# Kernel optimization log

Measured on AMD Instinct MI355X. Metric: run time of the kernel, lower is better.

Reference implementation:

```python
import jax, jax.numpy as jnp
import numpy as np

N = 100000   # nodes
E = 1280000  # edges (avg degree ~12.8)
D = 64       # feature / hidden channels


def _init_linear(key, fan_in, fan_out):
    # Kaiming-uniform-ish init like torch Linear
    bound = 1.0 / np.sqrt(fan_in)
    return jax.random.uniform(key, (fan_in, fan_out), minval=-bound, maxval=bound)


def setup_inputs() -> dict:
    key = jax.random.key(0)
    ks = jax.random.split(key, 16)
    inp = {
        "x": jax.random.normal(ks[0], (N, D), dtype=jnp.float32),
        "edge_index": jax.random.randint(ks[1], (2, E), 0, N, dtype=jnp.int32),
        "edge_weight": jax.random.uniform(ks[2], (E,), dtype=jnp.float32),
        "batch": jnp.zeros((N,), dtype=jnp.int32),
    }
    # GraphConv params per layer: lin_rel (weight+bias) applied to aggregated
    # neighbor sum, lin_root (weight, no bias) applied to the node itself.
    for i, k in zip((1, 2, 3), range(3, 12, 3)):
        inp[f"W_rel{i}"] = _init_linear(ks[k], D, D)
        inp[f"b_rel{i}"] = jnp.zeros((D,), dtype=jnp.float32)
        inp[f"W_root{i}"] = _init_linear(ks[k + 1], D, D)
    return inp


def _graph_conv(x, src, dst, w, W_rel, b_rel, W_root):
    # message: w_ij * x_j, aggregated (sum) at target nodes
    msg = w[:, None] * x[src]                                  # [E, D]
    agg = jax.ops.segment_sum(msg, dst, num_segments=N)       # [N, D]
    return agg @ W_rel + b_rel + x @ W_root                   # [N, D]


def reference(x, edge_index, edge_weight, batch,
              W_rel1, b_rel1, W_root1,
              W_rel2, b_rel2, W_root2,
              W_rel3, b_rel3, W_root3):
    src, dst = edge_index[0], edge_index[1]
    h = jax.nn.relu(_graph_conv(x, src, dst, edge_weight, W_rel1, b_rel1, W_root1))
    h = jax.nn.relu(_graph_conv(h, src, dst, edge_weight, W_rel2, b_rel2, W_root2))
    h = _graph_conv(h, src, dst, edge_weight, W_rel3, b_rel3, W_root3)
    return h
```

## Files before the change

### kernel.cpp

```cpp
#include <hip/hip_runtime.h>
#include <hip/hip_bf16.h>

#define NN 100000
#define NE 1280000
#define DD 64
#define RSHIFT 9
#define NRANGE 196
#define NPAD (NRANGE * 512)
#define RCAP 8192
#define RPSTRIDE 513

typedef __attribute__((ext_vector_type(8))) short bf16x8;
typedef __attribute__((ext_vector_type(4))) float f32x4;

static __device__ __forceinline__ unsigned short f2bf(float f) {
    __hip_bfloat16 h = __float2bfloat16(f);
    return *reinterpret_cast<unsigned short*>(&h);
}

__global__ __launch_bounds__(256) void f32_to_bf16_kernel(
    const float* __restrict__ in, unsigned short* __restrict__ out)
{
    int i = (blockIdx.x * 256 + threadIdx.x) * 4;
    float4 v = *(const float4*)(in + i);
    ushort4 o;
    o.x = f2bf(v.x); o.y = f2bf(v.y); o.z = f2bf(v.z); o.w = f2bf(v.w);
    *(ushort4*)(out + i) = o;
}

__global__ __launch_bounds__(256) void bpack_kernel(
    const float* __restrict__ Wrel1, const float* __restrict__ Wroot1,
    const float* __restrict__ Wrel2, const float* __restrict__ Wroot2,
    const float* __restrict__ Wrel3, const float* __restrict__ Wroot3,
    unsigned short* __restrict__ Bp, int* __restrict__ gcur)
{
    int L = blockIdx.x;
    int tid = threadIdx.x;
    if (L == 3) {
        if (tid < NRANGE) gcur[tid] = tid * RCAP;
        return;
    }
    const float* Wrel  = (L == 0) ? Wrel1  : (L == 1) ? Wrel2  : Wrel3;
    const float* Wroot = (L == 0) ? Wroot1 : (L == 1) ? Wroot2 : Wroot3;
    int wv = tid >> 6, lane = tid & 63, quad = lane >> 4, m16 = lane & 15;
    int n = wv * 16 + m16;
    unsigned short* o = Bp + (size_t)L * 4 * 256 * 8;
#pragma unroll
    for (int t = 0; t < 4; ++t)
#pragma unroll
        for (int j = 0; j < 8; ++j) {
            int k = t * 32 + quad * 8 + j;
            float wval = (k < 64) ? Wrel[k * 64 + n] : Wroot[(k - 64) * 64 + n];
            o[((size_t)t * 256 + tid) * 8 + j] = f2bf(wval);
        }
}

__global__ __launch_bounds__(512) void p1_bin_kernel(
    const int* __restrict__ src, const int* __restrict__ dst,
    const float* __restrict__ w, int* __restrict__ gcur,
    int2* __restrict__ ecoarse)
{
    __shared__ int2 stage[2048];
    __shared__ unsigned char sbkt[2048];
    __shared__ int cnt[NRANGE], ofs[NRANGE], gpos[NRANGE];
    __shared__ int wsum[4];

    int tid = threadIdx.x;
    int e0 = blockIdx.x * 2048 + tid * 4;
    int4   s4 = *(const int4*)(src + e0);
    int4   d4 = *(const int4*)(dst + e0);
    float4 w4 = *(const float4*)(w + e0);

    if (tid < NRANGE) cnt[tid] = 0;
    __syncthreads();

    int ss[4] = {s4.x, s4.y, s4.z, s4.w};
    int dd[4] = {d4.x, d4.y, d4.z, d4.w};
    float ww[4] = {w4.x, w4.y, w4.z, w4.w};
    int b[4], p[4];
#pragma unroll
    for (int i = 0; i < 4; ++i) {
        b[i] = dd[i] >> RSHIFT;
        p[i] = atomicAdd(&cnt[b[i]], 1);
    }
    __syncthreads();

    int sum = 0, v = 0;
    if (tid < NRANGE) {
        v = cnt[tid];
        int lane6 = tid & 63;
        sum = v;
#pragma unroll
        for (int o = 1; o < 64; o <<= 1) {
            int t = __shfl_up(sum, o);
            if (lane6 >= o) sum += t;
        }
        if (lane6 == 63 || tid == NRANGE - 1) wsum[tid >> 6] = sum;
        ofs[tid] = sum - v;
    }
    __syncthreads();
    if (tid < NRANGE) {
        int wid = tid >> 6;
        int pre = 0;
#pragma unroll
        for (int k = 0; k < 3; ++k) pre += (k < wid) ? wsum[k] : 0;
        ofs[tid] += pre;
        if (v > 0) gpos[tid] = atomicAdd(&gcur[tid], v);
    }
    __syncthreads();

#pragma unroll
    for (int i = 0; i < 4; ++i) {
        int slot = ofs[b[i]] + p[i];
        stage[slot] = make_int2(ss[i] | ((dd[i] & 511) << 17), __float_as_int(ww[i]));
        sbkt[slot] = (unsigned char)b[i];
    }
    __syncthreads();

#pragma unroll
    for (int u = 0; u < 4; ++u) {
        int j = tid + u * 512;
        int bb = sbkt[j];
        ecoarse[gpos[bb] + (j - ofs[bb])] = stage[j];
    }
}

__global__ __launch_bounds__(1024) void p2_place_kernel(
    const int2* __restrict__ ecoarse, const int* __restrict__ gcur,
    int* __restrict__ rowp, int2* __restrict__ ebuf)
{
    __shared__ int cnt[512];
    __shared__ int wsum[8];
    int r = blockIdx.x, tid = threadIdx.x;
    int beg = r * RCAP;
    int end = gcur[r];

    if (tid < 512) cnt[tid] = 0;
    __syncthreads();

    for (int j = beg + tid; j < end; j += 1024) {
        int2 rec = ecoarse[j];
        atomicAdd(&cnt[(rec.x >> 17) & 511], 1);
    }
    __syncthreads();

    int v = 0, sum = 0;
    if (tid < 512) {
        v = cnt[tid]; sum = v;
        int lane6 = tid & 63;
#pragma unroll
        for (int o = 1; o < 64; o <<= 1) {
            int t = __shfl_up(sum, o);
            if (lane6 >= o) sum += t;
        }
        if (lane6 == 63) wsum[tid >> 6] = sum;
    }
    __syncthreads();
    if (tid < 512) {
        int wid = tid >> 6;
        int pre = 0;
#pragma unroll
        for (int k = 0; k < 7; ++k) pre += (k < wid) ? wsum[k] : 0;
        int ex = beg + pre + sum - v;
        rowp[r * RPSTRIDE + tid] = ex;
        cnt[tid] = ex;
    }
    if (tid == 0) rowp[r * RPSTRIDE + 512] = end;
    __syncthreads();

    for (int j = beg + tid; j < end; j += 1024) {
        int2 rec = ecoarse[j];
        int dl = (rec.x >> 17) & 511;
        int pp = atomicAdd(&cnt[dl], 1);
        ebuf[pp] = make_int2((rec.x & 0x1FFFF) << 7, rec.y);
    }
}

template <bool RELU, bool OUT32>
__global__ __launch_bounds__(512) void fused_layer_kernel(
    const unsigned short* __restrict__ hb,
    const int* __restrict__ rowp,
    const int2* __restrict__ ebuf,
    const unsigned short* __restrict__ Bp,
    const float* __restrict__ brel,
    void* __restrict__ outp)
{
    __shared__ __align__(16) unsigned int AstW[4 * 256];
    __shared__ __align__(16) int2 seW[8][64];

    int tid = threadIdx.x;
    int lane = tid & 63;
    int wv = tid >> 6;
    int half = lane >> 5;
    int ch = lane & 31;
    int base = blockIdx.x * 16;
    int node = base + wv * 2 + half;
    int rr = base >> 9;

    const char* __restrict__ hbase = (const char*)hb;
    unsigned chB = (unsigned)ch * 4;

    bf16x8 bfrag[4];
    float bias = 0.f;
    if (wv < 4) {
#pragma unroll
        for (int t2 = 0; t2 < 4; ++t2)
            bfrag[t2] = *(const bf16x8*)(Bp + ((size_t)t2 * 256 + tid) * 8);
        bias = brel[(wv << 4) | (lane & 15)];
    }

    unsigned rootp = *(const unsigned*)(hbase + (size_t)node * 128 + chB);

    int beg = rowp[node + rr];
    int end = rowp[node + rr + 1];
    int deg = end - beg;

    float aL[4] = {0.f, 0.f, 0.f, 0.f};
    float aH[4] = {0.f, 0.f, 0.f, 0.f};

    for (int c = 0; c < deg; c += 32) {
        int nsl = deg - c; if (nsl > 32) nsl = 32;
        {
            int j = c + ch;
            bool ok = j < deg;
            int2 e = ebuf[beg + (ok ? j : (deg - 1))];
            if (!ok) e.y = 0;
            seW[wv][half * 32 + ch] = e;
        }
        for (int s0 = 0; s0 < nsl; s0 += 16) {
#pragma unroll
            for (int i = 0; i < 16; ++i) {
                int2 rec = seW[wv][half * 32 + s0 + i];
                float w = __int_as_float(rec.y);
                unsigned v = *(const unsigned*)(hbase + ((unsigned)rec.x + chB));
                aL[i & 3] = fmaf(w, __uint_as_float(v << 16), aL[i & 3]);
                aH[i & 3] = fmaf(w, __uint_as_float(v & 0xFFFF0000u), aH[i & 3]);
            }
        }
    }
    float accL = (aL[0] + aL[1]) + (aL[2] + aL[3]);
    float accH = (aH[0] + aH[1]) + (aH[2] + aH[3]);

    int m = wv * 2 + half;
    int t = ch >> 4, q = (ch >> 2) & 3, jj = ch & 3;
    unsigned pack = ((unsigned)f2bf(accH) << 16) | (unsigned)f2bf(accL);
    AstW[t * 256 + (q * 16 + m) * 4 + jj] = pack;
    AstW[(2 + t) * 256 + (q * 16 + m) * 4 + jj] = rootp;
    __syncthreads();

    if (wv < 4) {
        int quad = lane >> 4, m16 = lane & 15;
        int n = wv * 16 + m16;
        f32x4 cacc = {0.f, 0.f, 0.f, 0.f};
#pragma unroll
        for (int t2 = 0; t2 < 4; ++t2) {
            bf16x8 a = *(const bf16x8*)&AstW[t2 * 256 + lane * 4];
            cacc = __builtin_amdgcn_mfma_f32_16x16x32_bf16(a, bfrag[t2], cacc, 0, 0, 0);
        }
#pragma unroll
        for (int reg = 0; reg < 4; ++reg) {
            int row = quad * 4 + reg;
            size_t onode = (size_t)base + row;
            float v2 = cacc[reg] + bias;
            if (RELU) v2 = fmaxf(v2, 0.f);
            if (OUT32) ((float*)outp)[onode * DD + n] = v2;
            else       ((unsigned short*)outp)[onode * DD + n] = f2bf(v2);
        }
    }
}

extern "C" void kernel_launch(void* const* d_in, const int* in_sizes, int n_in,
                              void* d_out, int out_size, void* d_ws, size_t ws_size,
                              hipStream_t stream)
{
    const float* x     = (const float*)d_in[0];
    const int*   ei    = (const int*)d_in[1];
    const float* w     = (const float*)d_in[2];
    const float* Wrel1 = (const float*)d_in[4];
    const float* brel1 = (const float*)d_in[5];
    const float* Wroot1= (const float*)d_in[6];
    const float* Wrel2 = (const float*)d_in[7];
    const float* brel2 = (const float*)d_in[8];
    const float* Wroot2= (const float*)d_in[9];
    const float* Wrel3 = (const float*)d_in[10];
    const float* brel3 = (const float*)d_in[11];
    const float* Wroot3= (const float*)d_in[12];

    float* out = (float*)d_out;

    char* ws = (char*)d_ws;
    int2*  ebuf    = (int2*)ws;                ws += (size_t)NRANGE * RCAP * 8;
    int2*  ecoarse = (int2*)ws;
    unsigned short* xb  = (unsigned short*)ws; ws += (size_t)NRANGE * RCAP * 8;
    unsigned short* hb1 = (unsigned short*)ws; ws += (size_t)NPAD * DD * 2;
    unsigned short* hb2 = (unsigned short*)ws; ws += (size_t)NPAD * DD * 2;
    int*   rowp  = (int*)ws;                   ws += (size_t)(NRANGE * RPSTRIDE + 16) * 4;
    int*   gcur  = (int*)ws;                   ws += (size_t)256 * 4;
    unsigned short* Bp = (unsigned short*)ws;

    const int* src = ei;
    const int* dst = ei + NE;

    bpack_kernel<<<4, 256, 0, stream>>>(Wrel1, Wroot1, Wrel2, Wroot2,
                                        Wrel3, Wroot3, Bp, gcur);
    p1_bin_kernel<<<625, 512, 0, stream>>>(src, dst, w, gcur, ecoarse);
    p2_place_kernel<<<NRANGE, 1024, 0, stream>>>(ecoarse, gcur, rowp, ebuf);

    f32_to_bf16_kernel<<<6250, 256, 0, stream>>>(x, xb);

    fused_layer_kernel<true, false><<<NN / 16, 512, 0, stream>>>(
        xb, rowp, ebuf, Bp, brel1, hb1);
    fused_layer_kernel<true, false><<<NN / 16, 512, 0, stream>>>(
        hb1, rowp, ebuf, Bp + (size_t)4 * 256 * 8, brel2, hb2);
    fused_layer_kernel<false, true><<<NN / 16, 512, 0, stream>>>(
        hb2, rowp, ebuf, Bp + (size_t)8 * 256 * 8, brel3, out);
}
```

Measured before the change: 249.7 us.

## Process two nodes per half-wave and split MFMA epilogue across all eight waves

Result: slower. 277.3 us (+11.0%).

```diff
diff --git a/kernel.cpp b/kernel.cpp
--- a/kernel.cpp
+++ b/kernel.cpp
@@ -186,81 +186,98 @@
     void* __restrict__ outp)
 {
     __shared__ __align__(16) unsigned int AstW[4 * 256];
-    __shared__ __align__(16) int2 seW[8][64];
+    __shared__ __align__(16) int2 seW[8][2][64];
 
     int tid = threadIdx.x;
     int lane = tid & 63;
     int wv = tid >> 6;
     int half = lane >> 5;
     int ch = lane & 31;
-    int base = blockIdx.x * 16;
-    int node = base + wv * 2 + half;
+    int base = blockIdx.x * 32;
+    int m = wv * 2 + half;
+    int nodeA = base + m;
+    int nodeB = base + 16 + m;
     int rr = base >> 9;
 
     const char* __restrict__ hbase = (const char*)hb;
     unsigned chB = (unsigned)ch * 4;
 
+    int ti = wv >> 2, wv4 = wv & 3;
+    int quad = lane >> 4, m16 = lane & 15;
+
     bf16x8 bfrag[4];
-    float bias = 0.f;
-    if (wv < 4) {
-#pragma unroll
-        for (int t2 = 0; t2 < 4; ++t2)
-            bfrag[t2] = *(const bf16x8*)(Bp + ((size_t)t2 * 256 + tid) * 8);
-        bias = brel[(wv << 4) | (lane & 15)];
-    }
-
-    unsigned rootp = *(const unsigned*)(hbase + (size_t)node * 128 + chB);
-
-    int beg = rowp[node + rr];
-    int end = rowp[node + rr + 1];
-    int deg = end - beg;
-
-    float aL[4] = {0.f, 0.f, 0.f, 0.f};
-    float aH[4] = {0.f, 0.f, 0.f, 0.f};
-
-    for (int c = 0; c < deg; c += 32) {
-        int nsl = deg - c; if (nsl > 32) nsl = 32;
+#pragma unroll
+    for (int t2 = 0; t2 < 4; ++t2)
+        bfrag[t2] = *(const bf16x8*)(Bp + ((size_t)t2 * 256 + (tid & 255)) * 8);
+    float bias = brel[(wv4 << 4) | m16];
+    const char* rrow = hbase + (size_t)(base + ti * 16 + m16) * 128 + quad * 16;
+    bf16x8 aroot0 = *(const bf16x8*)(rrow);
+    bf16x8 aroot1 = *(const bf16x8*)(rrow + 64);
+
+    int begA = rowp[nodeA + rr];
+    int degA = rowp[nodeA + rr + 1] - begA;
+    int begB = rowp[nodeB + rr];
+    int degB = rowp[nodeB + rr + 1] - begB;
+    int dM = degA > degB ? degA : degB;
+
+    float aLA[4] = {0.f,0.f,0.f,0.f}, aHA[4] = {0.f,0.f,0.f,0.f};
+    float aLB[4] = {0.f,0.f,0.f,0.f}, aHB[4] = {0.f,0.f,0.f,0.f};
+
+    for (int c = 0; c < dM; c += 32) {
         {
             int j = c + ch;
-            bool ok = j < deg;
-            int2 e = ebuf[beg + (ok ? j : (deg - 1))];
-            if (!ok) e.y = 0;
-            seW[wv][half * 32 + ch] = e;
-        }
+            int ja = j < degA ? j : (degA - 1); if (ja < 0) ja = 0;
+            int jb = j < degB ? j : (degB - 1); if (jb < 0) jb = 0;
+            int2 eA = ebuf[begA + ja];
+            int2 eB = ebuf[begB + jb];
+            if (j >= degA) eA.y = 0;
+            if (j >= degB) eB.y = 0;
+            seW[wv][0][half * 32 + ch] = eA;
+            seW[wv][1][half * 32 + ch] = eB;
+        }
+        int nsl = dM - c; if (nsl > 32) nsl = 32;
         for (int s0 = 0; s0 < nsl; s0 += 16) {
 #pragma unroll
             for (int i = 0; i < 16; ++i) {
-                int2 rec = seW[wv][half * 32 + s0 + i];
-                float w = __int_as_float(rec.y);
-                unsigned v = *(const unsigned*)(hbase + ((unsigned)rec.x + chB));
-                aL[i & 3] = fmaf(w, __uint_as_float(v << 16), aL[i & 3]);
-                aH[i & 3] = fmaf(w, __uint_as_float(v & 0xFFFF0000u), aH[i & 3]);
+                int2 rA = seW[wv][0][half * 32 + s0 + i];
+                int2 rB = seW[wv][1][half * 32 + s0 + i];
+                float wA = __int_as_float(rA.y);
+                float wB = __int_as_float(rB.y);
+                unsigned vA = *(const unsigned*)(hbase + ((unsigned)rA.x + chB));
+                unsigned vB = *(const unsigned*)(hbase + ((unsigned)rB.x + chB));
+                aLA[i & 3] = fmaf(wA, __uint_as_float(vA << 16), aLA[i & 3]);
+                aHA[i & 3] = fmaf(wA, __uint_as_float(vA & 0xFFFF0000u), aHA[i & 3]);
+                aLB[i & 3] = fmaf(wB, __uint_as_float(vB << 16), aLB[i & 3]);
+                aHB[i & 3] = fmaf(wB, __uint_as_float(vB & 0xFFFF0000u), aHB[i & 3]);
             }
         }
     }
-    float accL = (aL[0] + aL[1]) + (aL[2] + aL[3]);
-    float accH = (aH[0] + aH[1]) + (aH[2] + aH[3]);
-
-    int m = wv * 2 + half;
+    float accLA = (aLA[0] + aLA[1]) + (aLA[2] + aLA[3]);
+    float accHA = (aHA[0] + aHA[1]) + (aHA[2] + aHA[3]);
+    float accLB = (aLB[0] + aLB[1]) + (aLB[2] + aLB[3]);
+    float accHB = (aHB[0] + aHB[1]) + (aHB[2] + aHB[3]);
+
     int t = ch >> 4, q = (ch >> 2) & 3, jj = ch & 3;
-    unsigned pack = ((unsigned)f2bf(accH) << 16) | (unsigned)f2bf(accL);
-    AstW[t * 256 + (q * 16 + m) * 4 + jj] = pack;
-    AstW[(2 + t) * 256 + (q * 16 + m) * 4 + jj] = rootp;
-    __syncthreads();
-
-    if (wv < 4) {
-        int quad = lane >> 4, m16 = lane & 15;
-        int n = wv * 16 + m16;
+    unsigned packA = ((unsigned)f2bf(accHA) << 16) | (unsigned)f2bf(accLA);
+    unsigned packB = ((unsigned)f2bf(accHB) << 16) | (unsigned)f2bf(accLB);
+    AstW[t * 256 + (q * 16 + m) * 4 + jj] = packA;
+    AstW[512 + t * 256 + (q * 16 + m) * 4 + jj] = packB;
+    __syncthreads();
+
+    {
+        int n = wv4 * 16 + m16;
         f32x4 cacc = {0.f, 0.f, 0.f, 0.f};
 #pragma unroll
-        for (int t2 = 0; t2 < 4; ++t2) {
-            bf16x8 a = *(const bf16x8*)&AstW[t2 * 256 + lane * 4];
+        for (int t2 = 0; t2 < 2; ++t2) {
+            bf16x8 a = *(const bf16x8*)&AstW[ti * 512 + t2 * 256 + lane * 4];
             cacc = __builtin_amdgcn_mfma_f32_16x16x32_bf16(a, bfrag[t2], cacc, 0, 0, 0);
         }
+        cacc = __builtin_amdgcn_mfma_f32_16x16x32_bf16(aroot0, bfrag[2], cacc, 0, 0, 0);
+        cacc = __builtin_amdgcn_mfma_f32_16x16x32_bf16(aroot1, bfrag[3], cacc, 0, 0, 0);
 #pragma unroll
         for (int reg = 0; reg < 4; ++reg) {
             int row = quad * 4 + reg;
-            size_t onode = (size_t)base + row;
+            size_t onode = (size_t)base + ti * 16 + row;
             float v2 = cacc[reg] + bias;
             if (RELU) v2 = fmaxf(v2, 0.f);
             if (OUT32) ((float*)outp)[onode * DD + n] = v2;
@@ -308,10 +325,10 @@
 
     f32_to_bf16_kernel<<<6250, 256, 0, stream>>>(x, xb);
 
-    fused_layer_kernel<true, false><<<NN / 16, 512, 0, stream>>>(
+    fused_layer_kernel<true, false><<<NN / 32, 512, 0, stream>>>(
         xb, rowp, ebuf, Bp, brel1, hb1);
-    fused_layer_kernel<true, false><<<NN / 16, 512, 0, stream>>>(
+    fused_layer_kernel<true, false><<<NN / 32, 512, 0, stream>>>(
         hb1, rowp, ebuf, Bp + (size_t)4 * 256 * 8, brel2, hb2);
-    fused_layer_kernel<false, true><<<NN / 16, 512, 0, stream>>>(
+    fused_layer_kernel<false, true><<<NN / 32, 512, 0, stream>>>(
         hb2, rowp, ebuf, Bp + (size_t)8 * 256 * 8, brel3, out);
 }
```
